# Kernel tuning notes

Measured on AMD Instinct MI355X. Metric: run time of the kernel, lower is better.

Reference implementation:

```python
import jax, jax.numpy as jnp
import numpy as np

VOCAB_SIZE = 62  # string.ascii_letters + string.digits
HIDDEN = 1024
STATE = int(HIDDEN * 4.0)  # state_size_mult=4.0
B, L = 2, 2048


def setup_inputs() -> dict:
    key = jax.random.key(0)
    ks = jax.random.split(key, 6)
    g = lambda k, shape, scale: (jax.random.normal(k, shape, jnp.float32) * scale)
    return {
        "tokens": jax.random.randint(ks[0], (B, L), 0, VOCAB_SIZE),
        "embed_w": g(ks[1], (VOCAB_SIZE, HIDDEN), 1.0),
        "norm_w": jnp.ones((HIDDEN,), jnp.float32),
        "in_w": g(ks[2], (HIDDEN, 4 * STATE), HIDDEN ** -0.5),
        "in_b": jnp.zeros((4 * STATE,), jnp.float32),
        "out_w": g(ks[3], (STATE, HIDDEN), STATE ** -0.5),
        "out_b": jnp.zeros((HIDDEN,), jnp.float32),
        "head_w": g(ks[4], (HIDDEN, VOCAB_SIZE), HIDDEN ** -0.5),
        "head_b": jnp.zeros((VOCAB_SIZE,), jnp.float32),
    }


def _rmsnorm(x, w, eps=1e-6):
    var = jnp.mean(x * x, axis=-1, keepdims=True)
    return x * jax.lax.rsqrt(var + eps) * w


def reference(tokens, embed_w, norm_w, in_w, in_b, out_w, out_b, head_w, head_b):
    # embedding lookup: [B, L, H]
    x = embed_w[tokens]
    res = x
    xn = _rmsnorm(x, norm_w)
    # single fused projection to (x_inner, a, b, c), each [B, L, STATE]
    proj = xn @ in_w + in_b
    xg, a_l, b_l, c_l = jnp.split(proj, 4, axis=-1)
    a = jax.nn.sigmoid(a_l)            # forget gate in (0,1)
    bx = jax.nn.sigmoid(b_l) * xg      # input contribution b_t * x_t
    # linear recurrence h_t = a_t * h_{t-1} + b_t * x_t via associative scan
    def comb(e1, e2):
        a1, h1 = e1
        a2, h2 = e2
        return a1 * a2, a2 * h1 + h2
    _, h = jax.lax.associative_scan(comb, (a, bx), axis=1)
    y = jax.nn.sigmoid(c_l) * h        # output gate c_t * h_t
    out = y @ out_w + out_b + res      # project back to hidden + residual
    return out @ head_w + head_b       # vocab logits [B, L, 62]
```

## Files before the change

kernel.cpp:

```cpp
#include <hip/hip_runtime.h>
#include <math.h>

#define HID   1024
#define STT   4096
#define MTOK  4096
#define LSEQ  2048
#define NCHUNK 64
#define CHUNK  32
#define VOCAB  62

typedef __attribute__((ext_vector_type(8))) short short8v;
typedef __attribute__((ext_vector_type(4))) float float4v;

typedef const __attribute__((address_space(1))) void* gptr_t;
typedef __attribute__((address_space(3))) void* lptr_t;

__device__ __forceinline__ float sigmoidf_(float x) {
    return 1.0f / (1.0f + __expf(-x));
}
__device__ __forceinline__ unsigned short f2bf(float f) {
    unsigned int u = __float_as_uint(f);
    unsigned int r = (u + 0x7fffu + ((u >> 16) & 1u)) >> 16;
    return (unsigned short)r;
}
__device__ __forceinline__ float bf2f(unsigned short b) {
    return __uint_as_float(((unsigned int)b) << 16);
}

__global__ __launch_bounds__(256) void fused_pre(
    const int* __restrict__ tokens, const float* __restrict__ embed_w,
    const float* __restrict__ norm_w, const float* __restrict__ in_w,
    const float* __restrict__ out_w, const float* __restrict__ head_w,
    const float* __restrict__ out_b, const float* __restrict__ head_b,
    unsigned short* __restrict__ in_wT, unsigned short* __restrict__ xn,
    unsigned short* __restrict__ W2T, float* __restrict__ E_head)
{
    __shared__ float sh[1056];
    int bid = blockIdx.x;
    int tid = threadIdx.x;
    if (bid < 16384) {
        float (*tile)[33] = (float (*)[33])sh;
        int c0 = (bid & 511) * 32, r0 = (bid >> 9) * 32;
        int r = tid >> 3, c4 = (tid & 7) << 2;
        float4 v = *(const float4*)(in_w + (size_t)(r0 + r) * 16384 + c0 + c4);
        tile[r][c4 + 0] = v.x; tile[r][c4 + 1] = v.y;
        tile[r][c4 + 2] = v.z; tile[r][c4 + 3] = v.w;
        __syncthreads();
        int oc = tid >> 3;
        int orr = (tid & 7) << 2;
        ushort4 o;
        o.x = f2bf(tile[orr + 0][oc]); o.y = f2bf(tile[orr + 1][oc]);
        o.z = f2bf(tile[orr + 2][oc]); o.w = f2bf(tile[orr + 3][oc]);
        *(ushort4*)(in_wT + (size_t)(c0 + oc) * 1024 + r0 + orr) = o;
    } else if (bid < 20480) {
        int m = bid - 16384;
        int tok = tokens[m];
        float4 x = ((const float4*)(embed_w + (size_t)tok * HID))[tid];
        float ss = x.x * x.x + x.y * x.y + x.z * x.z + x.w * x.w;
        for (int off = 32; off > 0; off >>= 1) ss += __shfl_down(ss, off);
        if ((tid & 63) == 0) sh[tid >> 6] = ss;
        __syncthreads();
        float tot = sh[0] + sh[1] + sh[2] + sh[3];
        float scale = rsqrtf(tot / (float)HID + 1e-6f);
        float4 w4 = ((const float4*)norm_w)[tid];
        ushort4 o;
        o.x = f2bf(x.x * scale * w4.x); o.y = f2bf(x.y * scale * w4.y);
        o.z = f2bf(x.z * scale * w4.z); o.w = f2bf(x.w * scale * w4.w);
        *(ushort4*)(xn + (size_t)m * HID + (tid << 2)) = o;
    } else if (bid < 21504) {
        float (*red)[4][64] = (float (*)[4][64])sh;
        int jc = tid >> 6, n = tid & 63;
        bool act = n < VOCAB;
        int k0 = (bid - 20480) * 4;
        float a[4] = {0.f, 0.f, 0.f, 0.f};
        int j0 = jc * 256;
        const float* w0 = out_w + (size_t)(k0 + 0) * HID;
        const float* w1 = out_w + (size_t)(k0 + 1) * HID;
        const float* w2 = out_w + (size_t)(k0 + 2) * HID;
        const float* w3 = out_w + (size_t)(k0 + 3) * HID;
        #pragma unroll 4
        for (int j = j0; j < j0 + 256; j++) {
            float h = act ? head_w[(size_t)j * VOCAB + n] : 0.f;
            a[0] = fmaf(w0[j], h, a[0]);
            a[1] = fmaf(w1[j], h, a[1]);
            a[2] = fmaf(w2[j], h, a[2]);
            a[3] = fmaf(w3[j], h, a[3]);
        }
        #pragma unroll
        for (int i = 0; i < 4; i++) red[jc][i][n] = a[i];
        __syncthreads();
        if (jc == 0) {
            #pragma unroll
            for (int i = 0; i < 4; i++) {
                float s = red[0][i][n] + red[1][i][n] + red[2][i][n] + red[3][i][n];
                W2T[(size_t)n * STT + k0 + i] = f2bf(s);
            }
        }
    } else {
        float (*red)[4][64] = (float (*)[4][64])sh;
        int jc = tid >> 6, n = tid & 63;
        bool act = n < VOCAB;
        int t = bid - 21504;
        const float* src = (t < VOCAB) ? (embed_w + (size_t)t * HID) : out_b;
        float acc = 0.f;
        if (act) {
            int j0 = jc * 256;
            #pragma unroll 4
            for (int j = j0; j < j0 + 256; j++)
                acc = fmaf(src[j], head_w[(size_t)j * VOCAB + n], acc);
        }
        red[jc][0][n] = acc;
        __syncthreads();
        if (tid < 64) {
            float s = red[0][0][n] + red[1][0][n] + red[2][0][n] + red[3][0][n];
            if (t == VOCAB && act) s += head_b[n];
            E_head[t * 64 + n] = s;
        }
    }
}

__global__ __launch_bounds__(512, 2) void gemm_in_mfma(
    const unsigned short* __restrict__ A, const unsigned short* __restrict__ B,
    const float* __restrict__ bias,
    unsigned short* __restrict__ a_out, unsigned short* __restrict__ bx_out,
    unsigned short* __restrict__ c_out,
    float* __restrict__ chunkA, float* __restrict__ chunkH)
{
    extern __shared__ unsigned short lds[];
    int tid = threadIdx.x;
    int wid = tid >> 6, lane = tid & 63;
    int wg = blockIdx.x;
    int xcd = wg & 7, loc = wg >> 3;
    int by = ((xcd >> 1) << 2) + (loc & 3);
    int bx = ((xcd & 1) << 5) + (loc >> 2);
    int m0 = by * 256, s0 = bx * 64;
    int wm = wid >> 2, wn = wid & 3;
    int lr = lane & 15, lk = lane >> 4;

    int cb0 = wid * 64, cb1 = 512 + wid * 64;
    int p0 = cb0 + lane, p1 = cb1 + lane;
    int row0 = p0 >> 2, ks0 = (p0 & 3) ^ ((row0 >> 1) & 3);
    int row1 = p1 >> 2, ks1 = (p1 & 3) ^ ((row1 >> 1) & 3);
    int arow0 = m0 + row0, arow1 = m0 + row1;
    int brow0 = ((row0 >> 6) << 12) + s0 + (row0 & 63);
    int brow1 = ((row1 >> 6) << 12) + s0 + (row1 & 63);

#define SHALF(grow0, grow1, b, which, kt, kk) do {                               \
    unsigned short* _d = lds + (b) * 32768 + (which) * 16384 + (kk) * 8192;      \
    __builtin_amdgcn_global_load_lds(                                            \
        (gptr_t)(const void*)(((which) ? B : A) + (size_t)(grow0) * 1024 +       \
                              (kt) * 64 + (kk) * 32 + ks0 * 8),                  \
        (lptr_t)(void*)(_d + (size_t)cb0 * 8), 16, 0, 0);                        \
    __builtin_amdgcn_global_load_lds(                                            \
        (gptr_t)(const void*)(((which) ? B : A) + (size_t)(grow1) * 1024 +       \
                              (kt) * 64 + (kk) * 32 + ks1 * 8),                  \
        (lptr_t)(void*)(_d + (size_t)cb1 * 8), 16, 0, 0);                        \
} while (0)

    int ksw = lk ^ ((lr >> 1) & 3);

#define RD_A(b, kk, mf) \
    (*(const short8v*)&lds[(b) * 32768 + (kk) * 8192 + \
        (((wm * 128 + (mf) * 16 + lr) << 2) + ksw) * 8])
#define RD_B(b, kk, nf) \
    (*(const short8v*)&lds[(b) * 32768 + 16384 + (kk) * 8192 + \
        ((((nf) * 64 + wn * 16 + lr) << 2) + ksw) * 8])

#define MFMA8x2(AF, B0, B1, n0i, n1i) do {                                       \
    __builtin_amdgcn_s_setprio(1);                                               \
    _Pragma("unroll")                                                            \
    for (int mf = 0; mf < 8; mf++) {                                             \
        acc[mf][n0i] = __builtin_amdgcn_mfma_f32_16x16x32_bf16(                  \
            (AF)[mf], (B0), acc[mf][n0i], 0, 0, 0);                              \
        acc[mf][n1i] = __builtin_amdgcn_mfma_f32_16x16x32_bf16(                  \
            (AF)[mf], (B1), acc[mf][n1i], 0, 0, 0);                              \
    }                                                                            \
    __builtin_amdgcn_s_setprio(0);                                               \
} while (0)

#define BAR_IN()  do { __builtin_amdgcn_s_barrier();                              \
    asm volatile("s_waitcnt lgkmcnt(0)" ::: "memory");                           \
    __builtin_amdgcn_sched_barrier(0); } while (0)
#define BAR_OUT() do { asm volatile("" ::: "memory");                             \
    __builtin_amdgcn_s_barrier(); } while (0)

    float4v acc[8][4];
    float4v z = {0.f, 0.f, 0.f, 0.f};
    #pragma unroll
    for (int i = 0; i < 8; i++)
        #pragma unroll
        for (int j = 0; j < 4; j++) acc[i][j] = z;

    SHALF(arow0, arow1, 0, 0, 0, 0); SHALF(brow0, brow1, 0, 1, 0, 0);
    SHALF(arow0, arow1, 0, 0, 0, 1); SHALF(brow0, brow1, 0, 1, 0, 1);
    asm volatile("s_waitcnt vmcnt(0)" ::: "memory");
    __builtin_amdgcn_s_barrier();

    short8v af[8], bf0, bf1;

    for (int kt = 0; kt < 16; ++kt) {
        int cur = kt & 1, nxt = cur ^ 1;
        int ktn = kt < 15 ? kt + 1 : 15;
        #pragma unroll
        for (int mf = 0; mf < 8; mf++) af[mf] = RD_A(cur, 0, mf);
        bf0 = RD_B(cur, 0, 0); bf1 = RD_B(cur, 0, 1);
        asm volatile("s_waitcnt vmcnt(4)" ::: "memory");
        SHALF(arow0, arow1, nxt, 0, ktn, 0);
        BAR_IN();
        MFMA8x2(af, bf0, bf1, 0, 1);
        BAR_OUT();
        bf0 = RD_B(cur, 0, 2); bf1 = RD_B(cur, 0, 3);
        SHALF(brow0, brow1, nxt, 1, ktn, 0);
        BAR_IN();
        MFMA8x2(af, bf0, bf1, 2, 3);
        BAR_OUT();
        #pragma unroll
        for (int mf = 0; mf < 8; mf++) af[mf] = RD_A(cur, 1, mf);
        bf0 = RD_B(cur, 1, 0); bf1 = RD_B(cur, 1, 1);
        asm volatile("s_waitcnt vmcnt(4)" ::: "memory");
        SHALF(arow0, arow1, nxt, 0, ktn, 1);
        BAR_IN();
        MFMA8x2(af, bf0, bf1, 0, 1);
        BAR_OUT();
        bf0 = RD_B(cur, 1, 2); bf1 = RD_B(cur, 1, 3);
        SHALF(brow0, brow1, nxt, 1, ktn, 1);
        BAR_IN();
        MFMA8x2(af, bf0, bf1, 2, 3);
        BAR_OUT();
    }

    int s = s0 + wn * 16 + lr;
    float b_xg = bias[s];
    float b_a  = bias[4096 + s];
    float b_b  = bias[8192 + s];
    float b_c  = bias[12288 + s];
    int rbase = lk << 2;
    int bb = m0 >> 11;
    int t0 = m0 & 2047;
    int ch = bb * STT + s;

    #pragma unroll
    for (int cc = 0; cc < 4; cc++) {
        float Afr[2], Hfr[2];
        #pragma unroll
        for (int e = 0; e < 2; e++) {
            int mf = cc * 2 + e;
            float Al = 1.f, Hl = 0.f;
            #pragma unroll
            for (int q = 0; q < 4; q++) {
                int m = m0 + wm * 128 + mf * 16 + rbase + q;
                size_t idx = (size_t)m * STT + s;
                float xg = acc[mf][0][q] + b_xg;
                float av = sigmoidf_(acc[mf][1][q] + b_a);
                float bxv = sigmoidf_(acc[mf][2][q] + b_b) * xg;
                float cv = sigmoidf_(acc[mf][3][q] + b_c);
                unsigned short au = f2bf(av), bu = f2bf(bxv);
                a_out[idx]  = au;
                bx_out[idx] = bu;
                c_out[idx]  = f2bf(cv);
                float ar = bf2f(au), br = bf2f(bu);
                Hl = fmaf(ar, Hl, br);
                Al = ar * Al;
            }
            #pragma unroll
            for (int d = 1; d <= 2; d <<= 1) {
                float Ap = __shfl(Al, lane - (d << 4));
                float Hp = __shfl(Hl, lane - (d << 4));
                if (lk >= d) { Hl = fmaf(Al, Hp, Hl); Al = Al * Ap; }
            }
            Afr[e] = Al; Hfr[e] = Hl;
        }
        if (lk == 3) {
            float Ac = Afr[1] * Afr[0];
            float Hc = fmaf(Afr[1], Hfr[0], Hfr[1]);
            int qg = (t0 >> 5) + wm * 4 + cc;
            chunkA[ch * NCHUNK + qg] = Ac;
            chunkH[ch * NCHUNK + qg] = Hc;
        }
    }
#undef SHALF
#undef RD_A
#undef RD_B
#undef MFMA8x2
#undef BAR_IN
#undef BAR_OUT
}

__global__ __launch_bounds__(256, 3) void logits_gemm(
    const unsigned short* __restrict__ Y, const unsigned short* __restrict__ W2T,
    float* __restrict__ part)
{
    extern __shared__ unsigned short lds[];
    int tid = threadIdx.x;
    int wid = tid >> 6, lane = tid & 63;
    int wg = blockIdx.x;
    int m0 = (wg & 31) * 128;
    int slice = wg >> 5;
    int ks0 = slice * 512;
    int wm = wid >> 1, wn = wid & 1;
    int lr = lane & 15, lk = lane >> 4;

    auto stage = [&](int b, int kt) {
        unsigned short* As = lds + b * 6144;
        unsigned short* Bs = As + 4096;
        #pragma unroll
        for (int i = 0; i < 2; i++) {
            int cb = i * 256 + wid * 64;
            int p = cb + lane;
            int row = p >> 2;
            int ks = (p & 3) ^ ((row >> 1) & 3);
            __builtin_amdgcn_global_load_lds(
                (gptr_t)(const void*)(Y + (size_t)(m0 + row) * STT + kt + ks * 8),
                (lptr_t)(void*)(As + (size_t)cb * 8), 16, 0, 0);
        }
        {
            int cb = wid * 64;
            int p = cb + lane;
            int row = p >> 2;
            int ks = (p & 3) ^ ((row >> 1) & 3);
            __builtin_amdgcn_global_load_lds(
                (gptr_t)(const void*)(W2T + (size_t)row * STT + kt + ks * 8),
                (lptr_t)(void*)(Bs + (size_t)cb * 8), 16, 0, 0);
        }
    };

    float4v acc[4][2];
    float4v z = {0.f, 0.f, 0.f, 0.f};
    #pragma unroll
    for (int i = 0; i < 4; i++) { acc[i][0] = z; acc[i][1] = z; }

    const int nt = 16;
    stage(0, ks0); stage(1, ks0 + 32);

    int ksw = lk ^ ((lr >> 1) & 3);

    for (int t = 0; t < nt; ++t) {
        if (t + 2 < nt) stage((t + 2) % 3, ks0 + (t + 2) * 32);
        if (t + 2 < nt)      asm volatile("s_waitcnt vmcnt(6)" ::: "memory");
        else if (t + 1 < nt) asm volatile("s_waitcnt vmcnt(3)" ::: "memory");
        else                 asm volatile("s_waitcnt vmcnt(0)" ::: "memory");
        __builtin_amdgcn_s_barrier();
        asm volatile("" ::: "memory");
        const unsigned short* As = lds + (t % 3) * 6144;
        const unsigned short* Bs = As + 4096;
        short8v af[4], bfr[2];
        #pragma unroll
        for (int f = 0; f < 4; f++)
            af[f] = *(const short8v*)&As[(((wm * 64 + f * 16 + lr) << 2) + ksw) * 8];
        #pragma unroll
        for (int g = 0; g < 2; g++)
            bfr[g] = *(const short8v*)&Bs[(((wn * 32 + g * 16 + lr) << 2) + ksw) * 8];
        __builtin_amdgcn_s_setprio(1);
        #pragma unroll
        for (int f = 0; f < 4; f++)
            #pragma unroll
            for (int g = 0; g < 2; g++)
                acc[f][g] = __builtin_amdgcn_mfma_f32_16x16x32_bf16(
                    af[f], bfr[g], acc[f][g], 0, 0, 0);
        __builtin_amdgcn_s_setprio(0);
        asm volatile("" ::: "memory");
        __builtin_amdgcn_s_barrier();
    }

    float* pb = part + (size_t)slice * MTOK * 64;
    int rbase = lk << 2;
    #pragma unroll
    for (int f = 0; f < 4; f++)
        #pragma unroll
        for (int g = 0; g < 2; g++) {
            int n = wn * 32 + g * 16 + lr;
            #pragma unroll
            for (int q = 0; q < 4; q++) {
                int m = m0 + wm * 64 + f * 16 + rbase + q;
                pb[(size_t)m * 64 + n] = acc[f][g][q];
            }
        }
}

__global__ __launch_bounds__(64) void logits_reduce(
    const float* __restrict__ part, const float* __restrict__ E_head,
    const int* __restrict__ tokens, float* __restrict__ logits)
{
    int m = blockIdx.x;
    int n = threadIdx.x;
    if (n >= VOCAB) return;
    int tok = tokens[m];
    float s = E_head[tok * 64 + n] + E_head[VOCAB * 64 + n];
    #pragma unroll
    for (int sl = 0; sl < 8; sl++)
        s += part[(size_t)sl * MTOK * 64 + (size_t)m * 64 + n];
    logits[(size_t)m * VOCAB + n] = s;
}

__global__ __launch_bounds__(256) void scan_phase2(
    const float* __restrict__ chunkA, const float* __restrict__ chunkH,
    float* __restrict__ carry)
{
    int ch = blockIdx.x * 256 + threadIdx.x;
    float c = 0.f;
    for (int q = 0; q < NCHUNK; q++) {
        carry[ch * NCHUNK + q] = c;
        c = fmaf(chunkA[ch * NCHUNK + q], c, chunkH[ch * NCHUNK + q]);
    }
}

__global__ __launch_bounds__(256) void scan_phase3(
    const unsigned short* __restrict__ a_buf, const unsigned short* __restrict__ bx_buf,
    const unsigned short* __restrict__ c_buf, const float* __restrict__ carry,
    unsigned short* __restrict__ y)
{
    int bid = blockIdx.x;
    int sg = bid & 3, q = (bid >> 2) & 63, b = bid >> 8;
    int s0 = sg * 1024 + threadIdx.x * 4;
    float h[4];
    #pragma unroll
    for (int j = 0; j < 4; j++)
        h[j] = carry[(b * STT + s0 + j) * NCHUNK + q];
    size_t base = (size_t)(b * LSEQ + q * CHUNK) * STT + s0;
    const unsigned short* ap = a_buf + base;
    const unsigned short* bp = bx_buf + base;
    const unsigned short* cp = c_buf + base;
    unsigned short* yp = y + base;
    for (int t = 0; t < CHUNK; t++) {
        ushort4 Av = *(const ushort4*)ap;
        ushort4 Bv = *(const ushort4*)bp;
        ushort4 Cv = *(const ushort4*)cp;
        const unsigned short* avp = (const unsigned short*)&Av;
        const unsigned short* bvp = (const unsigned short*)&Bv;
        const unsigned short* cvp = (const unsigned short*)&Cv;
        ushort4 o;
        unsigned short* op = (unsigned short*)&o;
        #pragma unroll
        for (int j = 0; j < 4; j++) {
            h[j] = fmaf(bf2f(avp[j]), h[j], bf2f(bvp[j]));
            op[j] = f2bf(bf2f(cvp[j]) * h[j]);
        }
        *(ushort4*)yp = o;
        ap += STT; bp += STT; cp += STT; yp += STT;
    }
}

extern "C" void kernel_launch(void* const* d_in, const int* in_sizes, int n_in,
                              void* d_out, int out_size, void* d_ws, size_t ws_size,
                              hipStream_t stream) {
    const int*   tokens  = (const int*)d_in[0];
    const float* embed_w = (const float*)d_in[1];
    const float* norm_w  = (const float*)d_in[2];
    const float* in_w    = (const float*)d_in[3];
    const float* in_b    = (const float*)d_in[4];
    const float* out_w   = (const float*)d_in[5];
    const float* out_b   = (const float*)d_in[6];
    const float* head_w  = (const float*)d_in[7];
    const float* head_b  = (const float*)d_in[8];
    float* logits = (float*)d_out;

    char* w = (char*)d_ws;
    unsigned short* a_buf  = (unsigned short*)w;
    unsigned short* bx_buf = (unsigned short*)(w + 33554432);
    unsigned short* c_buf  = (unsigned short*)(w + 67108864);
    unsigned short* W2T    = (unsigned short*)(w + 100663296);
    float*          E_head = (float*)(w + 101711872);
    float*          part   = (float*)(w + 102760448);
    unsigned short* y      = (unsigned short*)(w + 134217728);
    unsigned short* in_wT  = (unsigned short*)(w + 167772160);
    unsigned short* xn     = (unsigned short*)(w + 201326592);
    float* chunkA = (float*)(w + 209715200);
    float* chunkH = chunkA + 8192 * NCHUNK;
    float* carry  = chunkH + 8192 * NCHUNK;

    hipLaunchKernelGGL(fused_pre, dim3(16384 + 4096 + 1024 + VOCAB + 1), dim3(256), 0, stream,
                       tokens, embed_w, norm_w, in_w, out_w, head_w, out_b, head_b,
                       in_wT, xn, W2T, E_head);
    hipLaunchKernelGGL(gemm_in_mfma, dim3(1024), dim3(512), 131072, stream,
                       xn, in_wT, in_b, a_buf, bx_buf, c_buf, chunkA, chunkH);
    hipLaunchKernelGGL(scan_phase2, dim3(32), dim3(256), 0, stream,
                       chunkA, chunkH, carry);
    hipLaunchKernelGGL(scan_phase3, dim3(512), dim3(256), 0, stream,
                       a_buf, bx_buf, c_buf, carry, y);
    hipLaunchKernelGGL(logits_gemm, dim3(256), dim3(256), 36864, stream,
                       y, W2T, part);
    hipLaunchKernelGGL(logits_reduce, dim3(MTOK), dim3(64), 0, stream,
                       part, E_head, tokens, logits);
}
```

Before: 276.5 us.

## Fuse scan phase 3 into logits GEMM, keeping y tile in LDS

Merges the chunk-local scan replay with the output/logits GEMM. Each block now recomputes its 128-token by 128-state y tile from a, bx, c and the carries, writes it to LDS, and runs MFMAs against the W2T tile directly. This removes the round trip of the y buffer through global memory and one kernel launch. In exchange the grid drops to 256 blocks that alternate scan and MFMA with no double buffering, so the scan loads are serialized with the compute.

```diff
diff --git a/kernel.cpp b/kernel.cpp
--- a/kernel.cpp
+++ b/kernel.cpp
@@ -286,93 +286,124 @@
 #undef BAR_OUT
 }
 
-__global__ __launch_bounds__(256, 3) void logits_gemm(
-    const unsigned short* __restrict__ Y, const unsigned short* __restrict__ W2T,
-    float* __restrict__ part)
+__global__ __launch_bounds__(256) void scan_phase2(
+    const float* __restrict__ chunkA, const float* __restrict__ chunkH,
+    float* __restrict__ carry)
 {
-    extern __shared__ unsigned short lds[];
+    int ch = blockIdx.x * 256 + threadIdx.x;
+    float c = 0.f;
+    for (int q = 0; q < NCHUNK; q++) {
+        carry[ch * NCHUNK + q] = c;
+        c = fmaf(chunkA[ch * NCHUNK + q], c, chunkH[ch * NCHUNK + q]);
+    }
+}
+
+__global__ __launch_bounds__(256) void scan_logits(
+    const unsigned short* __restrict__ a_buf, const unsigned short* __restrict__ bx_buf,
+    const unsigned short* __restrict__ c_buf, const float* __restrict__ carry,
+    const unsigned short* __restrict__ W2T, float* __restrict__ part)
+{
+    __shared__ __align__(16) unsigned short y_lds[128 * 128];
+    __shared__ __align__(16) unsigned short b_lds[64 * 128];
     int tid = threadIdx.x;
-    int wid = tid >> 6, lane = tid & 63;
     int wg = blockIdx.x;
-    int m0 = (wg & 31) * 128;
-    int slice = wg >> 5;
-    int ks0 = slice * 512;
-    int wm = wid >> 1, wn = wid & 1;
+    int mt = wg & 31, sl = wg >> 5;
+    int m0 = mt * 128;
+    int bb = m0 >> 11;
+    int q0 = (m0 & 2047) >> 5;
+    int lane = tid & 63, wid = tid >> 6;
     int lr = lane & 15, lk = lane >> 4;
 
-    auto stage = [&](int b, int kt) {
-        unsigned short* As = lds + b * 6144;
-        unsigned short* Bs = As + 4096;
-        #pragma unroll
-        for (int i = 0; i < 2; i++) {
+    float4v acc[2][4];
+    float4v z = {0.f, 0.f, 0.f, 0.f};
+    #pragma unroll
+    for (int e = 0; e < 2; e++)
+        #pragma unroll
+        for (int nf = 0; nf < 4; nf++) acc[e][nf] = z;
+
+    for (int ks = 0; ks < 4; ++ks) {
+        int sbase = sl * 512 + ks * 128;
+        #pragma unroll
+        for (int i = 0; i < 4; i++) {
             int cb = i * 256 + wid * 64;
             int p = cb + lane;
-            int row = p >> 2;
-            int ks = (p & 3) ^ ((row >> 1) & 3);
+            int row = p >> 4, csw = p & 15;
+            int c = csw ^ (row & 7);
             __builtin_amdgcn_global_load_lds(
-                (gptr_t)(const void*)(Y + (size_t)(m0 + row) * STT + kt + ks * 8),
-                (lptr_t)(void*)(As + (size_t)cb * 8), 16, 0, 0);
+                (gptr_t)(const void*)(W2T + (size_t)row * STT + sbase + c * 8),
+                (lptr_t)(void*)(b_lds + (size_t)cb * 8), 16, 0, 0);
         }
         {
-            int cb = wid * 64;
-            int p = cb + lane;
-            int row = p >> 2;
-            int ks = (p & 3) ^ ((row >> 1) & 3);
-            __builtin_amdgcn_global_load_lds(
-                (gptr_t)(const void*)(W2T + (size_t)row * STT + kt + ks * 8),
-                (lptr_t)(void*)(Bs + (size_t)cb * 8), 16, 0, 0);
-        }
-    };
-
-    float4v acc[4][2];
-    float4v z = {0.f, 0.f, 0.f, 0.f};
-    #pragma unroll
-    for (int i = 0; i < 4; i++) { acc[i][0] = z; acc[i][1] = z; }
-
-    const int nt = 16;
-    stage(0, ks0); stage(1, ks0 + 32);
-
-    int ksw = lk ^ ((lr >> 1) & 3);
-
-    for (int t = 0; t < nt; ++t) {
-        if (t + 2 < nt) stage((t + 2) % 3, ks0 + (t + 2) * 32);
-        if (t + 2 < nt)      asm volatile("s_waitcnt vmcnt(6)" ::: "memory");
-        else if (t + 1 < nt) asm volatile("s_waitcnt vmcnt(3)" ::: "memory");
-        else                 asm volatile("s_waitcnt vmcnt(0)" ::: "memory");
-        __builtin_amdgcn_s_barrier();
-        asm volatile("" ::: "memory");
-        const unsigned short* As = lds + (t % 3) * 6144;
-        const unsigned short* Bs = As + 4096;
-        short8v af[4], bfr[2];
-        #pragma unroll
-        for (int f = 0; f < 4; f++)
-            af[f] = *(const short8v*)&As[(((wm * 64 + f * 16 + lr) << 2) + ksw) * 8];
-        #pragma unroll
-        for (int g = 0; g < 2; g++)
-            bfr[g] = *(const short8v*)&Bs[(((wn * 32 + g * 16 + lr) << 2) + ksw) * 8];
-        __builtin_amdgcn_s_setprio(1);
-        #pragma unroll
-        for (int f = 0; f < 4; f++)
-            #pragma unroll
-            for (int g = 0; g < 2; g++)
-                acc[f][g] = __builtin_amdgcn_mfma_f32_16x16x32_bf16(
-                    af[f], bfr[g], acc[f][g], 0, 0, 0);
-        __builtin_amdgcn_s_setprio(0);
-        asm volatile("" ::: "memory");
-        __builtin_amdgcn_s_barrier();
+            int chq = wid;
+            int s = sbase + lane * 2;
+            int q = q0 + chq;
+            size_t cidx = ((size_t)(bb * STT + s)) * NCHUNK + q;
+            float h0 = carry[cidx];
+            float h1 = carry[cidx + NCHUNK];
+            size_t gb = (size_t)(m0 + chq * 32) * STT + s;
+            const unsigned int* ap = (const unsigned int*)(a_buf + gb);
+            const unsigned int* bp = (const unsigned int*)(bx_buf + gb);
+            const unsigned int* cp = (const unsigned int*)(c_buf + gb);
+            const int stride = STT / 2;
+            #pragma unroll 4
+            for (int i = 0; i < 32; i++) {
+                unsigned int au = ap[(size_t)i * stride];
+                unsigned int bu = bp[(size_t)i * stride];
+                unsigned int cu = cp[(size_t)i * stride];
+                float a0 = bf2f((unsigned short)(au & 0xffff));
+                float a1 = bf2f((unsigned short)(au >> 16));
+                float b0 = bf2f((unsigned short)(bu & 0xffff));
+                float b1 = bf2f((unsigned short)(bu >> 16));
+                float c0 = bf2f((unsigned short)(cu & 0xffff));
+                float c1 = bf2f((unsigned short)(cu >> 16));
+                h0 = fmaf(a0, h0, b0);
+                h1 = fmaf(a1, h1, b1);
+                unsigned int yp = (unsigned int)f2bf(c0 * h0) |
+                                  ((unsigned int)f2bf(c1 * h1) << 16);
+                int row = chq * 32 + i;
+                int cw = (lane >> 2) ^ (row & 7);
+                *(unsigned int*)&y_lds[row * 128 + (cw << 3) + (lane & 3) * 2] = yp;
+            }
+        }
+        __syncthreads();
+        #pragma unroll
+        for (int kt2 = 0; kt2 < 4; kt2++) {
+            short8v af[2], bf[4];
+            #pragma unroll
+            for (int e = 0; e < 2; e++) {
+                int row = (wid * 2 + e) * 16 + lr;
+                int c = kt2 * 4 + lk;
+                af[e] = *(const short8v*)&y_lds[row * 128 + ((c ^ (row & 7)) << 3)];
+            }
+            #pragma unroll
+            for (int nf = 0; nf < 4; nf++) {
+                int row = nf * 16 + lr;
+                int c = kt2 * 4 + lk;
+                bf[nf] = *(const short8v*)&b_lds[row * 128 + ((c ^ (row & 7)) << 3)];
+            }
+            __builtin_amdgcn_s_setprio(1);
+            #pragma unroll
+            for (int e = 0; e < 2; e++)
+                #pragma unroll
+                for (int nf = 0; nf < 4; nf++)
+                    acc[e][nf] = __builtin_amdgcn_mfma_f32_16x16x32_bf16(
+                        af[e], bf[nf], acc[e][nf], 0, 0, 0);
+            __builtin_amdgcn_s_setprio(0);
+        }
+        __syncthreads();
     }
 
-    float* pb = part + (size_t)slice * MTOK * 64;
+    float* pb = part + (size_t)sl * MTOK * 64;
     int rbase = lk << 2;
     #pragma unroll
-    for (int f = 0; f < 4; f++)
-        #pragma unroll
-        for (int g = 0; g < 2; g++) {
-            int n = wn * 32 + g * 16 + lr;
+    for (int e = 0; e < 2; e++)
+        #pragma unroll
+        for (int nf = 0; nf < 4; nf++) {
+            int n = nf * 16 + lr;
             #pragma unroll
             for (int q = 0; q < 4; q++) {
-                int m = m0 + wm * 64 + f * 16 + rbase + q;
-                pb[(size_t)m * 64 + n] = acc[f][g][q];
+                int m = m0 + (wid * 2 + e) * 16 + rbase + q;
+                pb[(size_t)m * 64 + n] = acc[e][nf][q];
             }
         }
 }
@@ -392,54 +423,6 @@
     logits[(size_t)m * VOCAB + n] = s;
 }
 
-__global__ __launch_bounds__(256) void scan_phase2(
-    const float* __restrict__ chunkA, const float* __restrict__ chunkH,
-    float* __restrict__ carry)
-{
-    int ch = blockIdx.x * 256 + threadIdx.x;
-    float c = 0.f;
-    for (int q = 0; q < NCHUNK; q++) {
-        carry[ch * NCHUNK + q] = c;
-        c = fmaf(chunkA[ch * NCHUNK + q], c, chunkH[ch * NCHUNK + q]);
-    }
-}
-
-__global__ __launch_bounds__(256) void scan_phase3(
-    const unsigned short* __restrict__ a_buf, const unsigned short* __restrict__ bx_buf,
-    const unsigned short* __restrict__ c_buf, const float* __restrict__ carry,
-    unsigned short* __restrict__ y)
-{
-    int bid = blockIdx.x;
-    int sg = bid & 3, q = (bid >> 2) & 63, b = bid >> 8;
-    int s0 = sg * 1024 + threadIdx.x * 4;
-    float h[4];
-    #pragma unroll
-    for (int j = 0; j < 4; j++)
-        h[j] = carry[(b * STT + s0 + j) * NCHUNK + q];
-    size_t base = (size_t)(b * LSEQ + q * CHUNK) * STT + s0;
-    const unsigned short* ap = a_buf + base;
-    const unsigned short* bp = bx_buf + base;
-    const unsigned short* cp = c_buf + base;
-    unsigned short* yp = y + base;
-    for (int t = 0; t < CHUNK; t++) {
-        ushort4 Av = *(const ushort4*)ap;
-        ushort4 Bv = *(const ushort4*)bp;
-        ushort4 Cv = *(const ushort4*)cp;
-        const unsigned short* avp = (const unsigned short*)&Av;
-        const unsigned short* bvp = (const unsigned short*)&Bv;
-        const unsigned short* cvp = (const unsigned short*)&Cv;
-        ushort4 o;
-        unsigned short* op = (unsigned short*)&o;
-        #pragma unroll
-        for (int j = 0; j < 4; j++) {
-            h[j] = fmaf(bf2f(avp[j]), h[j], bf2f(bvp[j]));
-            op[j] = f2bf(bf2f(cvp[j]) * h[j]);
-        }
-        *(ushort4*)yp = o;
-        ap += STT; bp += STT; cp += STT; yp += STT;
-    }
-}
-
 extern "C" void kernel_launch(void* const* d_in, const int* in_sizes, int n_in,
                               void* d_out, int out_size, void* d_ws, size_t ws_size,
                               hipStream_t stream) {
@@ -461,7 +444,6 @@
     unsigned short* W2T    = (unsigned short*)(w + 100663296);
     float*          E_head = (float*)(w + 101711872);
     float*          part   = (float*)(w + 102760448);
-    unsigned short* y      = (unsigned short*)(w + 134217728);
     unsigned short* in_wT  = (unsigned short*)(w + 167772160);
     unsigned short* xn     = (unsigned short*)(w + 201326592);
     float* chunkA = (float*)(w + 209715200);
@@ -475,10 +457,8 @@
                        xn, in_wT, in_b, a_buf, bx_buf, c_buf, chunkA, chunkH);
     hipLaunchKernelGGL(scan_phase2, dim3(32), dim3(256), 0, stream,
                        chunkA, chunkH, carry);
-    hipLaunchKernelGGL(scan_phase3, dim3(512), dim3(256), 0, stream,
-                       a_buf, bx_buf, c_buf, carry, y);
-    hipLaunchKernelGGL(logits_gemm, dim3(256), dim3(256), 36864, stream,
-                       y, W2T, part);
+    hipLaunchKernelGGL(scan_logits, dim3(256), dim3(256), 0, stream,
+                       a_buf, bx_buf, c_buf, carry, W2T, part);
     hipLaunchKernelGGL(logits_reduce, dim3(MTOK), dim3(64), 0, stream,
                        part, E_head, tokens, logits);
 }
```

Result: faster. 265.2 us, median of 3 (-4.1%).
